# Performance work log

Hardware: AMD Instinct MI355X
Metric: run time of the kernel (lower is better)

The kernel has to match this reference:

```python
import jax, jax.numpy as jnp
import numpy as np

N, FIN, F, H = 4096, 128, 64, 8
NEG = -1e10


def setup_inputs() -> dict:
    key = jax.random.key(0)
    ks = jax.random.split(key, 6)
    X = jax.random.normal(ks[0], (N, FIN), dtype=jnp.float32)
    # sparse-ish binary adjacency with self loops, stored dense (as the layer expects)
    A = (jax.random.uniform(ks[1], (N, N)) < 0.05).astype(jnp.int32)
    A = A.at[jnp.arange(N), jnp.arange(N)].set(1)
    W = jax.random.normal(ks[2], (H, FIN, F), dtype=jnp.float32) * (1.0 / np.sqrt(FIN))
    b = jnp.zeros((H, F), dtype=jnp.float32)
    a_self = jax.random.normal(ks[3], (H, F), dtype=jnp.float32) * (1.0 / np.sqrt(F))
    a_neigh = jax.random.normal(ks[4], (H, F), dtype=jnp.float32) * (1.0 / np.sqrt(F))
    return {"X": X, "A": A, "W": W, "b": b, "a_self": a_self, "a_neigh": a_neigh}


def reference(X, A, W, b, a_self, a_neigh):
    # Dropout layers run in inference mode in the original call -> identity.
    feats = jnp.einsum('nf,hfo->hno', X, W)              # [H, N, F]
    s_self = jnp.einsum('hno,ho->hn', feats, a_self)     # [H, N]
    s_neigh = jnp.einsum('hno,ho->hn', feats, a_neigh)   # [H, N]
    scores = s_self[:, :, None] + s_neigh[:, None, :]    # [H, N, N]
    scores = jnp.where(scores > 0, scores, 0.2 * scores)  # LeakyReLU(0.2)
    mask = (1.0 - A.astype(jnp.float32)) * NEG            # [N, N]
    attn = jax.nn.softmax(scores + mask[None], axis=-1)   # [H, N, N]
    out = jnp.einsum('hnm,hmo->hno', attn, feats) + b[:, None, :]
    out = jax.nn.elu(out)                                 # [H, N, F]
    # concat heads -> [N, H*F]
    return jnp.transpose(out, (1, 0, 2)).reshape(N, H * F)
```

## Files before the change

kernel.cpp:

```cpp
#include <hip/hip_runtime.h>
#include <cmath>


#define NN 4096
#define FIN 128
#define FF 64
#define HH 8

typedef _Float16 h2 __attribute__((ext_vector_type(2)));
typedef _Float16 h4 __attribute__((ext_vector_type(4)));
typedef _Float16 h8 __attribute__((ext_vector_type(8)));
typedef float f32x2 __attribute__((ext_vector_type(2)));
typedef float f32x4 __attribute__((ext_vector_type(4)));

union H8 {
  h8 v;
  h2 p[4];
};
union U2 {
  h2 h;
  unsigned u;
};

static __device__ __forceinline__ float dot2acc(h2 a, float c) {
#if __has_builtin(__builtin_amdgcn_fdot2)
  return __builtin_amdgcn_fdot2(a, (h2){(_Float16)1.f, (_Float16)1.f}, c,
                                false);
#else
  return c + (float)a[0] + (float)a[1];
#endif
}

static __device__ __forceinline__ unsigned mask2(unsigned w, int j) {
#if __has_builtin(__builtin_amdgcn_sbfe) && __has_builtin(__builtin_amdgcn_perm)
  int lo = __builtin_amdgcn_sbfe((int)w, j, 1);
  int hi = __builtin_amdgcn_sbfe((int)w, j + 1, 1);
  return __builtin_amdgcn_perm((unsigned)hi, (unsigned)lo, 0x05040100u);
#else
  int lo = ((int)(w << (31 - j))) >> 31;
  int hi = ((int)(w << (30 - j))) >> 31;
  return ((unsigned)lo & 0xFFFFu) | ((unsigned)hi << 16);
#endif
}

static __device__ __forceinline__ void gload16(const void* g, void* l) {
  __builtin_amdgcn_global_load_lds(
      (const __attribute__((address_space(1))) unsigned int*)g,
      (__attribute__((address_space(3))) unsigned int*)l, 16, 0, 0);
}

__global__ __launch_bounds__(256) void pack_kernel(
    const int* __restrict__ A, const float* __restrict__ W,
    const float* __restrict__ X, unsigned long long* __restrict__ bits,
    _Float16* __restrict__ Wsw, _Float16* __restrict__ Xsw) {
  const int b = blockIdx.x;
  const int tid = threadIdx.x;
  const int wave = tid >> 6, lane = tid & 63;
  if (b < NN) {
    __shared__ int ldsT[4][4][256];
    const int* ar = A + (size_t)b * NN;
    int4 v[4];
#pragma unroll
    for (int it = 0; it < 4; ++it) {
      const int g = wave * 4 + it;
      v[it] = *(const int4*)(ar + g * 256 + lane * 4);
    }
#pragma unroll
    for (int it = 0; it < 4; ++it) *(int4*)&ldsT[wave][it][lane * 4] = v[it];
    unsigned long long* br = bits + ((size_t)b << 6);
#pragma unroll
    for (int it = 0; it < 4; ++it) {
      const int g = wave * 4 + it;
      int w0 = ldsT[wave][it][0 * 64 + lane];
      int w1 = ldsT[wave][it][1 * 64 + lane];
      int w2 = ldsT[wave][it][2 * 64 + lane];
      int w3 = ldsT[wave][it][3 * 64 + lane];
      unsigned long long m0 = __ballot(w0 != 0);
      unsigned long long m1 = __ballot(w1 != 0);
      unsigned long long m2 = __ballot(w2 != 0);
      unsigned long long m3 = __ballot(w3 != 0);
      if (lane == 0) {
        ulonglong2 p0 = {m0, m1}, p1 = {m2, m3};
        *(ulonglong2*)(br + g * 4 + 0) = p0;
        *(ulonglong2*)(br + g * 4 + 2) = p1;
      }
    }
  } else if (b < NN + 2) {
    const int h0 = (b - NN) * 4;
    for (int h = h0; h < h0 + 4; ++h) {
      for (int c = tid; c < 1024; c += 256) {
        int ln = c & 63, nb = (c >> 6) & 3, kt = c >> 8;
        int f = nb * 16 + (ln & 15);
        int k0 = kt * 32 + (ln >> 4) * 8;
        h8 v;
#pragma unroll
        for (int j = 0; j < 8; ++j)
          v[j] = (_Float16)W[((size_t)(h * FIN) + k0 + j) * FF + f];
        *(h8*)(Wsw + ((size_t)(((h * 4 + kt) * 4 + nb) * 64 + ln)) * 8) = v;
      }
    }
  } else {
    const int tile = (b - NN - 2) * 4 + wave;
    const int l16 = lane & 15, quad = lane >> 4;
    const float* xr = X + (size_t)(tile * 16 + l16) * FIN;
#pragma unroll
    for (int kt = 0; kt < 4; ++kt) {
      int k0 = kt * 32 + quad * 8;
      f32x4 x0 = *(const f32x4*)(xr + k0);
      f32x4 x1 = *(const f32x4*)(xr + k0 + 4);
      h8 v = {(_Float16)x0[0], (_Float16)x0[1], (_Float16)x0[2],
              (_Float16)x0[3], (_Float16)x1[0], (_Float16)x1[1],
              (_Float16)x1[2], (_Float16)x1[3]};
      *(h8*)(Xsw + ((size_t)((tile * 4 + kt) * 64 + lane)) * 8) = v;
    }
  }
}

__global__ __launch_bounds__(256) void feats_kernel(
    const _Float16* __restrict__ Xsw, const _Float16* __restrict__ Wsw,
    const float* __restrict__ a_self, const float* __restrict__ a_neigh,
    _Float16* __restrict__ feats_sw, _Float16* __restrict__ es_h,
    _Float16* __restrict__ esn_h, _Float16* __restrict__ et_h,
    _Float16* __restrict__ etn_h) {
  const int h = blockIdx.y;
  const int tid = threadIdx.x, wave = tid >> 6, lane = tid & 63;
  const int l16 = lane & 15, quad = lane >> 4;
  const int rt = blockIdx.x * 4 + wave;
  const int r0 = rt * 16;

  f32x4 acc[4];
#pragma unroll
  for (int nb = 0; nb < 4; ++nb) acc[nb] = (f32x4){0.f, 0.f, 0.f, 0.f};

  const _Float16* xp = Xsw + ((size_t)(rt * 4) * 64 + lane) * 8;
  const _Float16* wp = Wsw + ((size_t)(h * 16) * 64 + lane) * 8;
  h8 Af[4];
#pragma unroll
  for (int kt = 0; kt < 4; ++kt) Af[kt] = *(const h8*)(xp + kt * 512);
#pragma unroll
  for (int kt = 0; kt < 4; ++kt)
#pragma unroll
    for (int nb = 0; nb < 4; ++nb) {
      h8 Bf = *(const h8*)(wp + (kt * 4 + nb) * 512);
      acc[nb] = __builtin_amdgcn_mfma_f32_16x16x32_f16(Af[kt], Bf, acc[nb], 0, 0, 0);
    }

  float as[4], an[4];
#pragma unroll
  for (int nb = 0; nb < 4; ++nb) {
    as[nb] = a_self[h * FF + nb * 16 + l16];
    an[nb] = a_neigh[h * FF + nb * 16 + l16];
  }
#pragma unroll
  for (int r = 0; r < 4; ++r) {
    float ps = acc[0][r] * as[0] + acc[1][r] * as[1] + acc[2][r] * as[2] +
               acc[3][r] * as[3];
    float pn = acc[0][r] * an[0] + acc[1][r] * an[1] + acc[2][r] * an[2] +
               acc[3][r] * an[3];
#pragma unroll
    for (int m = 1; m <= 8; m <<= 1) {
      ps += __shfl_xor(ps, m, 64);
      pn += __shfl_xor(pn, m, 64);
    }
    if (l16 == 0) {
      int node = h * NN + r0 + quad * 4 + r;
      es_h[node] = (_Float16)__expf(ps - 2.0f);
      esn_h[node] = (_Float16)__expf(0.2f * ps - 2.0f);
      et_h[node] = (_Float16)__expf(pn - 2.0f);
      etn_h[node] = (_Float16)__expf(0.2f * pn - 2.0f);
    }
  }

  const int kb = r0 >> 5;
  const int quadA = ((r0 >> 4) & 1) * 2 + (quad >> 1);
  const int jbase = (quad & 1) << 2;
#pragma unroll
  for (int nb = 0; nb < 4; ++nb) {
    h4 v = {(_Float16)acc[nb][0], (_Float16)acc[nb][1], (_Float16)acc[nb][2],
            (_Float16)acc[nb][3]};
    size_t off = ((size_t)((h * 128 + kb) * 4 + nb) << 9) +
                 ((quadA * 16 + l16) << 3) + jbase;
    *(h4*)(feats_sw + off) = v;
  }
}

__global__ __launch_bounds__(512, 4) void attn_kernel(
    const unsigned long long* __restrict__ Abits,
    const _Float16* __restrict__ feats_sw, const _Float16* __restrict__ es_h,
    const _Float16* __restrict__ esn_h, const _Float16* __restrict__ et_h,
    const _Float16* __restrict__ etn_h, const float* __restrict__ bias,
    float* __restrict__ out) {
  const int bid = blockIdx.x;
  const int h = bid & 7, n0 = (bid >> 3) << 6;
  const int tid = threadIdx.x, wave = tid >> 6, lane = tid & 63;
  const int l16 = lane & 15, quad = lane >> 4;
  const int shq = quad << 3;
  const int rtile = wave & 3, half = wave >> 2;

  __shared__ __align__(16) char smem[3 * 19456];

  const int myrow = n0 + (rtile << 4) + l16;
  _Float16 e = es_h[h * NN + myrow];
  _Float16 en = esn_h[h * NN + myrow];
  const h2 esp = (h2){e, e};
  const h2 esnp = (h2){en, en};

  f32x4 acc[4];
#pragma unroll
  for (int nb = 0; nb < 4; ++nb) acc[nb] = (f32x4){0.f, 0.f, 0.f, 0.f};
  float dsA = 0.f, dsB = 0.f;

  const char* gF = (const char*)feats_sw + ((size_t)h << 19);
  const char* gE = (const char*)et_h + (h << 13);
  const char* gEN = (const char*)etn_h + (h << 13);
  const char* gB = (const char*)Abits + ((size_t)n0 << 9);

#define STAGE(s_, bw_)                                                         \
  do {                                                                         \
    char* L_ = smem + (bw_)*19456;                                             \
    const char* src_ = gF + ((size_t)(s_) << 14) + (wave << 11) + (lane << 4); \
    gload16(src_, L_ + (wave << 11) + (lane << 4));                            \
    gload16(src_ + 1024, L_ + (wave << 11) + 1024 + (lane << 4));              \
    if (wave == 0)                                                             \
      gload16(gE + ((s_) << 8) + (l16 << 4), L_ + 16384 + (lane << 4));        \
    if (wave == 1)                                                             \
      gload16(gEN + ((s_) << 8) + (l16 << 4), L_ + 17408 + (lane << 4));       \
    if (wave == 2)                                                             \
      gload16(gB + ((size_t)lane << 9) + ((s_) << 4), L_ + 18432 + (lane << 4)); \
  } while (0)

  STAGE(0, 0);
  STAGE(1, 1);

  for (int s = 0; s < 32; ++s) {
    __builtin_amdgcn_sched_barrier(0);
    if (s < 31) {
      if (wave < 3)
        asm volatile("s_waitcnt vmcnt(3)" ::: "memory");
      else
        asm volatile("s_waitcnt vmcnt(2)" ::: "memory");
    } else {
      asm volatile("s_waitcnt vmcnt(0)" ::: "memory");
    }
    __builtin_amdgcn_sched_barrier(0);
    __builtin_amdgcn_s_barrier();
    if (s < 30) STAGE(s + 2, (s + 2) % 3);

    const char* L = smem + (s % 3) * 19456;
    unsigned long long myb = *(const unsigned long long*)(
        L + 18432 + (((rtile << 4) + l16) << 4) + (half << 3));
#pragma unroll
    for (int kf = 0; kf < 2; ++kf) {
      H8 ET, ETN;
      ET.v = *(const h8*)(L + 16384 + (half << 7) + (kf << 6) + (quad << 4));
      ETN.v = *(const h8*)(L + 17408 + (half << 7) + (kf << 6) + (quad << 4));
      const char* fB = L + (half << 13) + (kf << 12) + (lane << 4);
      h8 B0 = *(const h8*)(fB);
      h8 B1 = *(const h8*)(fB + 1024);
      h8 B2 = *(const h8*)(fB + 2048);
      h8 B3 = *(const h8*)(fB + 3072);
      unsigned wsw = (unsigned)(myb >> (kf ? 32 : 0)) >> shq;
      H8 P;
#pragma unroll
      for (int p = 0; p < 4; ++p) {
        h2 a_ = esp * ET.p[p];
        h2 b_ = esnp * ETN.p[p];
        h2 r_ = __builtin_elementwise_max(a_, b_);
        U2 u_;
        u_.h = r_;
        u_.u &= mask2(wsw, 2 * p);
        P.p[p] = u_.h;
        if (p & 1)
          dsB = dot2acc(u_.h, dsB);
        else
          dsA = dot2acc(u_.h, dsA);
      }
      acc[0] = __builtin_amdgcn_mfma_f32_16x16x32_f16(P.v, B0, acc[0], 0, 0, 0);
      acc[1] = __builtin_amdgcn_mfma_f32_16x16x32_f16(P.v, B1, acc[1], 0, 0, 0);
      acc[2] = __builtin_amdgcn_mfma_f32_16x16x32_f16(P.v, B2, acc[2], 0, 0, 0);
      acc[3] = __builtin_amdgcn_mfma_f32_16x16x32_f16(P.v, B3, acc[3], 0, 0, 0);
    }
  }
#undef STAGE

  float den = dsA + dsB;
  den += __shfl_xor(den, 16, 64);
  den += __shfl_xor(den, 32, 64);

  float(*accL)[16][68] = (float(*)[16][68])smem;
  float(*denL)[16] = (float(*)[16])(smem + 4 * 16 * 68 * 4);
  __syncthreads();
  if (half == 1) {
#pragma unroll
    for (int nb = 0; nb < 4; ++nb)
#pragma unroll
      for (int r = 0; r < 4; ++r)
        accL[rtile][quad * 4 + r][nb * 16 + l16] = acc[nb][r];
    if (quad == 0) denL[rtile][l16] = den;
  }
  __syncthreads();
  if (half == 0) {
    float dtot = den + denL[rtile][l16];
    const int orow = n0 + (rtile << 4) + (quad << 2);
#pragma unroll
    for (int r = 0; r < 4; ++r) {
      float dr = __shfl(dtot, (quad << 2) + r, 64);
      float inv = 1.0f / dr;
#pragma unroll
      for (int nb = 0; nb < 4; ++nb) {
        float x = (acc[nb][r] + accL[rtile][quad * 4 + r][nb * 16 + l16]) * inv +
                  bias[h * FF + nb * 16 + l16];
        x = x > 0.f ? x : (__expf(x) - 1.0f);
        out[(size_t)(orow + r) * (HH * FF) + h * FF + nb * 16 + l16] = x;
      }
    }
  }
}

extern "C" void kernel_launch(void* const* d_in, const int* in_sizes, int n_in,
                              void* d_out, int out_size, void* d_ws,
                              size_t ws_size, hipStream_t stream) {
  const float* X = (const float*)d_in[0];
  const int* A = (const int*)d_in[1];
  const float* W = (const float*)d_in[2];
  const float* b = (const float*)d_in[3];
  const float* a_self = (const float*)d_in[4];
  const float* a_neigh = (const float*)d_in[5];
  float* out = (float*)d_out;

  char* ws = (char*)d_ws;
  unsigned long long* Abits = (unsigned long long*)ws;
  _Float16* feats_sw = (_Float16*)(ws + (2u << 20));
  _Float16* es_h = (_Float16*)(ws + (6u << 20));
  _Float16* esn_h = (_Float16*)(ws + (6u << 20) + (64u << 10));
  _Float16* et_h = (_Float16*)(ws + (6u << 20) + (128u << 10));
  _Float16* etn_h = (_Float16*)(ws + (6u << 20) + (192u << 10));
  _Float16* Wsw = (_Float16*)(ws + (6u << 20) + (256u << 10));
  _Float16* Xsw = (_Float16*)(ws + (6u << 20) + (384u << 10));

  pack_kernel<<<NN + 66, 256, 0, stream>>>(A, W, X, Abits, Wsw, Xsw);
  feats_kernel<<<dim3(64, 8), 256, 0, stream>>>(Xsw, Wsw, a_self, a_neigh,
                                                feats_sw, es_h, esn_h, et_h,
                                                etn_h);
  attn_kernel<<<512, 512, 0, stream>>>(Abits, feats_sw, es_h, esn_h, et_h,
                                       etn_h, b, out);
}
```

Baseline: 144.8 us.

## Repartition attention waves over row pairs and compute softmax denominators via MFMA

Waves now split work by row-half, column-half and k-fragment, so each wave handles two 16-row tiles that reuse the same feature B fragments and ET/ETN loads from LDS. The per-element fdot2 denominator accumulation is replaced by an extra MFMA against a ones vector, moving that sum onto the matrix unit. The epilogue becomes a four-way cross-wave reduction through LDS with vectorized float4 output stores, done in two passes. The aim is to cut LDS reads and VALU work per MFMA, at the cost of more accumulator registers and an extra MFMA per tile.

Result: no change. 143.9 us (-0.6%).

```diff
diff --git a/kernel.cpp b/kernel.cpp
--- a/kernel.cpp
+++ b/kernel.cpp
@@ -21,15 +21,6 @@
   h2 h;
   unsigned u;
 };
-
-static __device__ __forceinline__ float dot2acc(h2 a, float c) {
-#if __has_builtin(__builtin_amdgcn_fdot2)
-  return __builtin_amdgcn_fdot2(a, (h2){(_Float16)1.f, (_Float16)1.f}, c,
-                                false);
-#else
-  return c + (float)a[0] + (float)a[1];
-#endif
-}
 
 static __device__ __forceinline__ unsigned mask2(unsigned w, int j) {
 #if __has_builtin(__builtin_amdgcn_sbfe) && __has_builtin(__builtin_amdgcn_perm)
@@ -195,20 +186,29 @@
   const int tid = threadIdx.x, wave = tid >> 6, lane = tid & 63;
   const int l16 = lane & 15, quad = lane >> 4;
   const int shq = quad << 3;
-  const int rtile = wave & 3, half = wave >> 2;
+  const int rh = wave & 1, ctw = (wave >> 1) & 1, kfw = wave >> 2;
 
   __shared__ __align__(16) char smem[3 * 19456];
 
-  const int myrow = n0 + (rtile << 4) + l16;
-  _Float16 e = es_h[h * NN + myrow];
-  _Float16 en = esn_h[h * NN + myrow];
-  const h2 esp = (h2){e, e};
-  const h2 esnp = (h2){en, en};
-
-  f32x4 acc[4];
-#pragma unroll
-  for (int nb = 0; nb < 4; ++nb) acc[nb] = (f32x4){0.f, 0.f, 0.f, 0.f};
-  float dsA = 0.f, dsB = 0.f;
+  h2 esp[2], esnp[2];
+#pragma unroll
+  for (int rt = 0; rt < 2; ++rt) {
+    const int myrow = n0 + (rh << 5) + (rt << 4) + l16;
+    _Float16 e = es_h[h * NN + myrow];
+    _Float16 en = esn_h[h * NN + myrow];
+    esp[rt] = (h2){e, e};
+    esnp[rt] = (h2){en, en};
+  }
+
+  f32x4 acc[2][4], accd[2];
+#pragma unroll
+  for (int rt = 0; rt < 2; ++rt) {
+    accd[rt] = (f32x4){0.f, 0.f, 0.f, 0.f};
+#pragma unroll
+    for (int nb = 0; nb < 4; ++nb) acc[rt][nb] = (f32x4){0.f, 0.f, 0.f, 0.f};
+  }
+  const h8 ONES = {(_Float16)1.f, (_Float16)1.f, (_Float16)1.f, (_Float16)1.f,
+                   (_Float16)1.f, (_Float16)1.f, (_Float16)1.f, (_Float16)1.f};
 
   const char* gF = (const char*)feats_sw + ((size_t)h << 19);
   const char* gE = (const char*)et_h + (h << 13);
@@ -247,73 +247,83 @@
     if (s < 30) STAGE(s + 2, (s + 2) % 3);
 
     const char* L = smem + (s % 3) * 19456;
-    unsigned long long myb = *(const unsigned long long*)(
-        L + 18432 + (((rtile << 4) + l16) << 4) + (half << 3));
-#pragma unroll
-    for (int kf = 0; kf < 2; ++kf) {
-      H8 ET, ETN;
-      ET.v = *(const h8*)(L + 16384 + (half << 7) + (kf << 6) + (quad << 4));
-      ETN.v = *(const h8*)(L + 17408 + (half << 7) + (kf << 6) + (quad << 4));
-      const char* fB = L + (half << 13) + (kf << 12) + (lane << 4);
-      h8 B0 = *(const h8*)(fB);
-      h8 B1 = *(const h8*)(fB + 1024);
-      h8 B2 = *(const h8*)(fB + 2048);
-      h8 B3 = *(const h8*)(fB + 3072);
-      unsigned wsw = (unsigned)(myb >> (kf ? 32 : 0)) >> shq;
+    unsigned long long mb0 = *(const unsigned long long*)(
+        L + 18432 + (((rh << 5) + l16) << 4) + (ctw << 3));
+    unsigned long long mb1 = *(const unsigned long long*)(
+        L + 18432 + (((rh << 5) + 16 + l16) << 4) + (ctw << 3));
+    H8 ET, ETN;
+    ET.v = *(const h8*)(L + 16384 + (ctw << 7) + (kfw << 6) + (quad << 4));
+    ETN.v = *(const h8*)(L + 17408 + (ctw << 7) + (kfw << 6) + (quad << 4));
+    const char* fB = L + (ctw << 13) + (kfw << 12) + (lane << 4);
+    h8 B0 = *(const h8*)(fB);
+    h8 B1 = *(const h8*)(fB + 1024);
+    h8 B2 = *(const h8*)(fB + 2048);
+    h8 B3 = *(const h8*)(fB + 3072);
+
+#pragma unroll
+    for (int rt = 0; rt < 2; ++rt) {
+      unsigned long long myb = rt ? mb1 : mb0;
+      unsigned wsw = (unsigned)(myb >> (kfw ? 32 : 0)) >> shq;
       H8 P;
 #pragma unroll
       for (int p = 0; p < 4; ++p) {
-        h2 a_ = esp * ET.p[p];
-        h2 b_ = esnp * ETN.p[p];
+        h2 a_ = esp[rt] * ET.p[p];
+        h2 b_ = esnp[rt] * ETN.p[p];
         h2 r_ = __builtin_elementwise_max(a_, b_);
         U2 u_;
         u_.h = r_;
         u_.u &= mask2(wsw, 2 * p);
         P.p[p] = u_.h;
-        if (p & 1)
-          dsB = dot2acc(u_.h, dsB);
-        else
-          dsA = dot2acc(u_.h, dsA);
       }
-      acc[0] = __builtin_amdgcn_mfma_f32_16x16x32_f16(P.v, B0, acc[0], 0, 0, 0);
-      acc[1] = __builtin_amdgcn_mfma_f32_16x16x32_f16(P.v, B1, acc[1], 0, 0, 0);
-      acc[2] = __builtin_amdgcn_mfma_f32_16x16x32_f16(P.v, B2, acc[2], 0, 0, 0);
-      acc[3] = __builtin_amdgcn_mfma_f32_16x16x32_f16(P.v, B3, acc[3], 0, 0, 0);
+      acc[rt][0] =
+          __builtin_amdgcn_mfma_f32_16x16x32_f16(P.v, B0, acc[rt][0], 0, 0, 0);
+      acc[rt][1] =
+          __builtin_amdgcn_mfma_f32_16x16x32_f16(P.v, B1, acc[rt][1], 0, 0, 0);
+      acc[rt][2] =
+          __builtin_amdgcn_mfma_f32_16x16x32_f16(P.v, B2, acc[rt][2], 0, 0, 0);
+      acc[rt][3] =
+          __builtin_amdgcn_mfma_f32_16x16x32_f16(P.v, B3, acc[rt][3], 0, 0, 0);
+      accd[rt] =
+          __builtin_amdgcn_mfma_f32_16x16x32_f16(P.v, ONES, accd[rt], 0, 0, 0);
     }
   }
 #undef STAGE
 
-  float den = dsA + dsB;
-  den += __shfl_xor(den, 16, 64);
-  den += __shfl_xor(den, 32, 64);
-
   float(*accL)[16][68] = (float(*)[16][68])smem;
-  float(*denL)[16] = (float(*)[16])(smem + 4 * 16 * 68 * 4);
-  __syncthreads();
-  if (half == 1) {
+  float* denL = (float*)(smem + 8 * 16 * 68 * 4);
+  const int erow = tid >> 4;
+  const int rh_o = erow >> 4, r16 = erow & 15;
+  const int ec0 = (tid & 15) << 2;
+#pragma unroll
+  for (int rt = 0; rt < 2; ++rt) {
+    __syncthreads();
 #pragma unroll
     for (int nb = 0; nb < 4; ++nb)
 #pragma unroll
       for (int r = 0; r < 4; ++r)
-        accL[rtile][quad * 4 + r][nb * 16 + l16] = acc[nb][r];
-    if (quad == 0) denL[rtile][l16] = den;
-  }
-  __syncthreads();
-  if (half == 0) {
-    float dtot = den + denL[rtile][l16];
-    const int orow = n0 + (rtile << 4) + (quad << 2);
-#pragma unroll
-    for (int r = 0; r < 4; ++r) {
-      float dr = __shfl(dtot, (quad << 2) + r, 64);
-      float inv = 1.0f / dr;
-#pragma unroll
-      for (int nb = 0; nb < 4; ++nb) {
-        float x = (acc[nb][r] + accL[rtile][quad * 4 + r][nb * 16 + l16]) * inv +
-                  bias[h * FF + nb * 16 + l16];
-        x = x > 0.f ? x : (__expf(x) - 1.0f);
-        out[(size_t)(orow + r) * (HH * FF) + h * FF + nb * 16 + l16] = x;
-      }
-    }
+        accL[wave][quad * 4 + r][nb * 16 + l16] = acc[rt][nb][r];
+    if (l16 == 0) {
+#pragma unroll
+      for (int r = 0; r < 4; ++r) denL[wave * 16 + quad * 4 + r] = accd[rt][r];
+    }
+    __syncthreads();
+    f32x4 v = (f32x4){0.f, 0.f, 0.f, 0.f};
+    float dn = 0.f;
+#pragma unroll
+    for (int cw = 0; cw < 4; ++cw) {
+      const int w = rh_o + ((cw & 1) << 1) + ((cw >> 1) << 2);
+      v += *(const f32x4*)&accL[w][r16][ec0];
+      dn += denL[w * 16 + r16];
+    }
+    float inv = 1.0f / dn;
+    const f32x4 bv = *(const f32x4*)(bias + h * FF + ec0);
+#pragma unroll
+    for (int i = 0; i < 4; ++i) {
+      float x = v[i] * inv + bv[i];
+      v[i] = x > 0.f ? x : (__expf(x) - 1.0f);
+    }
+    *(f32x4*)(out + (size_t)(n0 + (rh_o << 5) + (rt << 4) + r16) * (HH * FF) +
+              h * FF + ec0) = v;
   }
 }
 
```
